# Kernel optimization log

Measured on AMD Instinct MI355X. Metric: run time of the kernel, lower is better.

The kernel has to match this reference:

```python
import jax, jax.numpy as jnp
import numpy as np

N_NODES = 100000


def _gcn_layer(x, src, dst, W, b, n_nodes):
    # x: [N, Cin]; src/dst already include self-loops
    h = x @ W  # [N, Cout]
    deg = jax.ops.segment_sum(jnp.ones_like(dst, dtype=h.dtype), dst,
                              num_segments=n_nodes)  # in-degree incl. self-loop
    dinv = jnp.where(deg > 0, deg ** -0.5, 0.0)
    norm = dinv[src] * dinv[dst]  # [E]
    msg = h[src] * norm[:, None]  # [E, Cout]
    out = jax.ops.segment_sum(msg, dst, num_segments=n_nodes)
    return out + b


def setup_inputs() -> dict:
    key = jax.random.key(0)
    k1, k2, k3, k4, k5, k6, k7 = jax.random.split(key, 7)
    E = 6400000
    x = jax.random.normal(k1, (N_NODES, 5), dtype=jnp.float32)
    edge_index = jax.random.randint(k2, (2, E), 0, N_NODES, dtype=jnp.int64)
    edge_f = jax.random.normal(k3, (E,), dtype=jnp.float32)
    edge_attr = jax.random.normal(k4, (E, 1), dtype=jnp.float32)
    # GCNConv params (glorot-ish scale)
    W1 = jax.random.normal(k5, (5, 8), dtype=jnp.float32) * (1.0 / np.sqrt(5))
    b1 = jnp.zeros((8,), dtype=jnp.float32)
    W2 = jax.random.normal(k6, (8, 5), dtype=jnp.float32) * (1.0 / np.sqrt(8))
    b2 = jnp.zeros((5,), dtype=jnp.float32)
    return {"x": x, "edge_index": edge_index, "edge_f": edge_f,
            "edge_attr": edge_attr, "W1": W1, "b1": b1, "W2": W2, "b2": b2}


def reference(x, edge_index, edge_f, edge_attr, W1, b1, W2, b2):
    n = x.shape[0]
    loops = jnp.arange(n, dtype=edge_index.dtype)
    src = jnp.concatenate([edge_index[0], loops])  # add self-loops (PyG default)
    dst = jnp.concatenate([edge_index[1], loops])
    h = _gcn_layer(x, src, dst, W1, b1, n)
    h = _gcn_layer(h, src, dst, W2, b2, n)
    return h
```

## Files before the change

### kernel.cpp

```cpp
#include <hip/hip_runtime.h>
#include <hip/hip_fp16.h>


#define TPB 256
#define VPB 256
#define B_BITS 8
#define MAXB 512
#define CAP 17408
#define NBLK_E 512
#define EPB 12500
#define SCT 512

typedef int int4e __attribute__((ext_vector_type(4)));
typedef _Float16 h8 __attribute__((ext_vector_type(8)));

__device__ __forceinline__ int4e ntload4(const int* p) {
    return __builtin_nontemporal_load((const int4e*)p);
}
__device__ __forceinline__ int ntload(const int* p) {
    return __builtin_nontemporal_load(p);
}

__global__ void k_init(int B, int* __restrict__ bpos) {
    int b = blockIdx.x * blockDim.x + threadIdx.x;
    if (b < B) bpos[b] = b * CAP;
}

__global__ __launch_bounds__(SCT) void k_scat(const int* __restrict__ src,
        const int* __restrict__ dst, int E, int B,
        int* __restrict__ bpos, int* __restrict__ pairs) {
    __shared__ int sorted[EPB];
    __shared__ int hist[MAXB], scn[MAXB], cur[MAXB], gbase[MAXB];
    int t = threadIdx.x;
    for (int i = t; i < MAXB; i += SCT) hist[i] = 0;
    __syncthreads();
    int lo = blockIdx.x * EPB;
    int n = min(E - lo, EPB);
    int n4 = n & ~3;
    for (int i = t * 4; i < n4; i += SCT * 4) {
        int4e d4 = ntload4(dst + lo + i);
        atomicAdd(&hist[d4.x >> B_BITS], 1);
        atomicAdd(&hist[d4.y >> B_BITS], 1);
        atomicAdd(&hist[d4.z >> B_BITS], 1);
        atomicAdd(&hist[d4.w >> B_BITS], 1);
    }
    for (int i = n4 + t; i < n; i += SCT)
        atomicAdd(&hist[dst[lo + i] >> B_BITS], 1);
    __syncthreads();
    if (t < MAXB) scn[t] = hist[t];
    __syncthreads();
    for (int off = 1; off < MAXB; off <<= 1) {
        int v = (t >= off && t < MAXB) ? scn[t - off] : 0;
        __syncthreads();
        if (t < MAXB) scn[t] += v;
        __syncthreads();
    }
    if (t < MAXB) {
        int h = hist[t];
        cur[t] = scn[t] - h;
        gbase[t] = (t < B && h) ? atomicAdd(&bpos[t], h) : 0;
    }
    __syncthreads();
    for (int i = t * 4; i < n4; i += SCT * 4) {
        int4e d4 = ntload4(dst + lo + i);
        int4e s4 = ntload4(src + lo + i);
        int p;
        p = atomicAdd(&cur[d4.x >> B_BITS], 1); sorted[p] = (s4.x << B_BITS) | (d4.x & (VPB - 1));
        p = atomicAdd(&cur[d4.y >> B_BITS], 1); sorted[p] = (s4.y << B_BITS) | (d4.y & (VPB - 1));
        p = atomicAdd(&cur[d4.z >> B_BITS], 1); sorted[p] = (s4.z << B_BITS) | (d4.z & (VPB - 1));
        p = atomicAdd(&cur[d4.w >> B_BITS], 1); sorted[p] = (s4.w << B_BITS) | (d4.w & (VPB - 1));
    }
    for (int i = n4 + t; i < n; i += SCT) {
        int d = dst[lo + i], s = src[lo + i];
        int p = atomicAdd(&cur[d >> B_BITS], 1);
        sorted[p] = (s << B_BITS) | (d & (VPB - 1));
    }
    __syncthreads();
    int wave = t >> 6, lane = t & 63;
    for (int bb = wave; bb < B; bb += (SCT >> 6)) {
        int h = hist[bb];
        int st = scn[bb] - h;
        int gb = gbase[bb];
        for (int j = lane; j < h; j += 64)
            pairs[gb + j] = sorted[st + j];
    }
}

__global__ __launch_bounds__(1024) void k_pre(int* __restrict__ pairs,
        const int* __restrict__ bpos, const float* __restrict__ x,
        unsigned int* __restrict__ jinfo, _Float16* __restrict__ xs, int N) {
    __shared__ int csr[CAP];
    __shared__ int hist[VPB], cur[VPB];
    __shared__ int scn[VPB];
    int t = threadIdx.x, b = blockIdx.x;
    if (t < VPB) hist[t] = 0;
    __syncthreads();
    int base = b * CAP;
    int n = bpos[b] - base, n4 = n & ~3;
    for (int i = t * 4; i < n4; i += 1024 * 4) {
        int4e p = ntload4(pairs + base + i);
        atomicAdd(&hist[p.x & (VPB - 1)], 1);
        atomicAdd(&hist[p.y & (VPB - 1)], 1);
        atomicAdd(&hist[p.z & (VPB - 1)], 1);
        atomicAdd(&hist[p.w & (VPB - 1)], 1);
    }
    for (int i = n4 + t; i < n; i += 1024)
        atomicAdd(&hist[pairs[base + i] & (VPB - 1)], 1);
    __syncthreads();
    if (t < VPB) scn[t] = hist[t];
    __syncthreads();
    for (int off = 1; off < VPB; off <<= 1) {
        int v = (t >= off && t < VPB) ? scn[t - off] : 0;
        __syncthreads();
        if (t < VPB) scn[t] += v;
        __syncthreads();
    }
    int node = b * VPB + t;
    if (t < VPB) {
        int h = hist[t];
        int sl = scn[t] - h;
        cur[t] = sl;
        if (node < N) {
            jinfo[node] = ((unsigned int)(base + sl) << 9) | (unsigned int)h;
            float di = rsqrtf((float)(h + 1));
            const float* xp = x + (size_t)node * 5;
            h8 v;
            v[0] = (_Float16)(xp[0] * di); v[1] = (_Float16)(xp[1] * di);
            v[2] = (_Float16)(xp[2] * di); v[3] = (_Float16)(xp[3] * di);
            v[4] = (_Float16)(xp[4] * di);
            v[5] = (_Float16)0.f; v[6] = (_Float16)0.f; v[7] = (_Float16)0.f;
            *(h8*)(xs + (size_t)node * 8) = v;
        }
    }
    __syncthreads();
    for (int i = t * 4; i < n4; i += 1024 * 4) {
        int4e p = ntload4(pairs + base + i);
        int q;
        q = atomicAdd(&cur[p.x & (VPB - 1)], 1); csr[q] = p.x >> B_BITS;
        q = atomicAdd(&cur[p.y & (VPB - 1)], 1); csr[q] = p.y >> B_BITS;
        q = atomicAdd(&cur[p.z & (VPB - 1)], 1); csr[q] = p.z >> B_BITS;
        q = atomicAdd(&cur[p.w & (VPB - 1)], 1); csr[q] = p.w >> B_BITS;
    }
    for (int i = n4 + t; i < n; i += 1024) {
        int p = pairs[base + i];
        int q = atomicAdd(&cur[p & (VPB - 1)], 1);
        csr[q] = p >> B_BITS;
    }
    __syncthreads();
    for (int i = t; i < n; i += 1024)
        __builtin_nontemporal_store(csr[i], pairs + base + i);
}

__global__ __launch_bounds__(TPB) void k_g1(const int* __restrict__ pairs,
        const unsigned int* __restrict__ jinfo, const _Float16* __restrict__ xs,
        const float* __restrict__ W1, const float* __restrict__ b1,
        const float* __restrict__ W2, _Float16* __restrict__ h2s, int N) {
    int gid = blockIdx.x * blockDim.x + threadIdx.x;
    int node = gid >> 3, lane = gid & 7;
    if (node >= N) return;
    unsigned int u = jinfo[node];
    int jsa = (int)(u >> 9), cn = (int)(u & 511u);
    float a0 = 0.f, a1 = 0.f, a2 = 0.f, a3 = 0.f, a4 = 0.f;
    int j = lane;
    for (; j + 24 < cn; j += 32) {
        int sA = ntload(pairs + jsa + j);
        int sB = ntload(pairs + jsa + j + 8);
        int sC = ntload(pairs + jsa + j + 16);
        int sD = ntload(pairs + jsa + j + 24);
        h8 vA = *(const h8*)(xs + (size_t)sA * 8);
        h8 vB = *(const h8*)(xs + (size_t)sB * 8);
        h8 vC = *(const h8*)(xs + (size_t)sC * 8);
        h8 vD = *(const h8*)(xs + (size_t)sD * 8);
        a0 += (float)vA[0] + (float)vB[0] + (float)vC[0] + (float)vD[0];
        a1 += (float)vA[1] + (float)vB[1] + (float)vC[1] + (float)vD[1];
        a2 += (float)vA[2] + (float)vB[2] + (float)vC[2] + (float)vD[2];
        a3 += (float)vA[3] + (float)vB[3] + (float)vC[3] + (float)vD[3];
        a4 += (float)vA[4] + (float)vB[4] + (float)vC[4] + (float)vD[4];
    }
    for (; j < cn; j += 8) {
        int sA = ntload(pairs + jsa + j);
        h8 vA = *(const h8*)(xs + (size_t)sA * 8);
        a0 += (float)vA[0]; a1 += (float)vA[1]; a2 += (float)vA[2];
        a3 += (float)vA[3]; a4 += (float)vA[4];
    }
#pragma unroll
    for (int d = 1; d < 8; d <<= 1) {
        a0 += __shfl_xor(a0, d); a1 += __shfl_xor(a1, d);
        a2 += __shfl_xor(a2, d); a3 += __shfl_xor(a3, d);
        a4 += __shfl_xor(a4, d);
    }
    float di = rsqrtf((float)(cn + 1));
    h8 sv = *(const h8*)(xs + (size_t)node * 8);
    float tc[5];
    tc[0] = a0 + (float)sv[0]; tc[1] = a1 + (float)sv[1];
    tc[2] = a2 + (float)sv[2]; tc[3] = a3 + (float)sv[3];
    tc[4] = a4 + (float)sv[4];
    float o1[8];
#pragma unroll
    for (int jj = 0; jj < 8; ++jj) {
        float h = 0.f;
#pragma unroll
        for (int c = 0; c < 5; ++c) h += tc[c] * W1[c * 8 + jj];
        o1[jj] = h * di + b1[jj];
    }
    if (lane == 0) {
        h8 w;
#pragma unroll
        for (int k = 0; k < 5; ++k) {
            float h = 0.f;
#pragma unroll
            for (int jj = 0; jj < 8; ++jj) h += o1[jj] * W2[jj * 5 + k];
            w[k] = (_Float16)(h * di);
        }
        w[5] = (_Float16)0.f; w[6] = (_Float16)0.f; w[7] = (_Float16)0.f;
        *(h8*)(h2s + (size_t)node * 8) = w;
    }
}

__global__ __launch_bounds__(TPB) void k_g2(const int* __restrict__ pairs,
        const unsigned int* __restrict__ jinfo, const _Float16* __restrict__ h2s,
        const float* __restrict__ b2, float* __restrict__ out, int N) {
    int gid = blockIdx.x * blockDim.x + threadIdx.x;
    int node = gid >> 3, lane = gid & 7;
    if (node >= N) return;
    unsigned int u = jinfo[node];
    int jsa = (int)(u >> 9), cn = (int)(u & 511u);
    float a0 = 0.f, a1 = 0.f, a2 = 0.f, a3 = 0.f, a4 = 0.f;
    int j = lane;
    for (; j + 24 < cn; j += 32) {
        int sA = ntload(pairs + jsa + j);
        int sB = ntload(pairs + jsa + j + 8);
        int sC = ntload(pairs + jsa + j + 16);
        int sD = ntload(pairs + jsa + j + 24);
        h8 vA = *(const h8*)(h2s + (size_t)sA * 8);
        h8 vB = *(const h8*)(h2s + (size_t)sB * 8);
        h8 vC = *(const h8*)(h2s + (size_t)sC * 8);
        h8 vD = *(const h8*)(h2s + (size_t)sD * 8);
        a0 += (float)vA[0] + (float)vB[0] + (float)vC[0] + (float)vD[0];
        a1 += (float)vA[1] + (float)vB[1] + (float)vC[1] + (float)vD[1];
        a2 += (float)vA[2] + (float)vB[2] + (float)vC[2] + (float)vD[2];
        a3 += (float)vA[3] + (float)vB[3] + (float)vC[3] + (float)vD[3];
        a4 += (float)vA[4] + (float)vB[4] + (float)vC[4] + (float)vD[4];
    }
    for (; j < cn; j += 8) {
        int sA = ntload(pairs + jsa + j);
        h8 vA = *(const h8*)(h2s + (size_t)sA * 8);
        a0 += (float)vA[0]; a1 += (float)vA[1]; a2 += (float)vA[2];
        a3 += (float)vA[3]; a4 += (float)vA[4];
    }
#pragma unroll
    for (int d = 1; d < 8; d <<= 1) {
        a0 += __shfl_xor(a0, d); a1 += __shfl_xor(a1, d);
        a2 += __shfl_xor(a2, d); a3 += __shfl_xor(a3, d);
        a4 += __shfl_xor(a4, d);
    }
    if (lane == 0) {
        float di = rsqrtf((float)(cn + 1));
        h8 sv = *(const h8*)(h2s + (size_t)node * 8);
        float* op = out + (size_t)node * 5;
        op[0] = (a0 + (float)sv[0]) * di + b2[0];
        op[1] = (a1 + (float)sv[1]) * di + b2[1];
        op[2] = (a2 + (float)sv[2]) * di + b2[2];
        op[3] = (a3 + (float)sv[3]) * di + b2[3];
        op[4] = (a4 + (float)sv[4]) * di + b2[4];
    }
}

extern "C" void kernel_launch(void* const* d_in, const int* in_sizes, int n_in,
                              void* d_out, int out_size, void* d_ws, size_t ws_size,
                              hipStream_t stream) {
    const float* x   = (const float*)d_in[0];
    const int*  eidx = (const int*)d_in[1];
    const float* W1 = (const float*)d_in[4];
    const float* b1 = (const float*)d_in[5];
    const float* W2 = (const float*)d_in[6];
    const float* b2 = (const float*)d_in[7];
    float* out = (float*)d_out;

    const int N = in_sizes[0] / 5;
    const int E = in_sizes[1] / 2;
    const int* src = eidx;
    const int* dst = eidx + E;

    const int B = (N + VPB - 1) / VPB;

    int*      pairs = (int*)d_ws;
    _Float16* xs    = (_Float16*)(pairs + (size_t)B * CAP);
    _Float16* h2s   = xs + (size_t)8 * N;
    unsigned int* jinfo = (unsigned int*)(h2s + (size_t)8 * N);
    int*      bpos  = (int*)(jinfo + N);

    const int g8N = (8 * N + TPB - 1) / TPB;

    k_init <<<(B + TPB - 1) / TPB, TPB, 0, stream>>>(B, bpos);
    k_scat <<<NBLK_E, SCT, 0, stream>>>(src, dst, E, B, bpos, pairs);
    k_pre  <<<B, 1024, 0, stream>>>(pairs, bpos, x, jinfo, xs, N);
    k_g1   <<<g8N, TPB, 0, stream>>>(pairs, jinfo, xs, W1, b1, W2, h2s, N);
    k_g2   <<<g8N, TPB, 0, stream>>>(pairs, jinfo, h2s, b2, out, N);
}
```

Measured before the change: 255.4 us.

## Drop nontemporal hints, prefetch gather indices, and remap blocks to interleave node buckets

```diff
diff --git a/kernel.cpp b/kernel.cpp
--- a/kernel.cpp
+++ b/kernel.cpp
@@ -14,11 +14,8 @@
 typedef int int4e __attribute__((ext_vector_type(4)));
 typedef _Float16 h8 __attribute__((ext_vector_type(8)));
 
-__device__ __forceinline__ int4e ntload4(const int* p) {
-    return __builtin_nontemporal_load((const int4e*)p);
-}
-__device__ __forceinline__ int ntload(const int* p) {
-    return __builtin_nontemporal_load(p);
+__device__ __forceinline__ int4e ld4(const int* p) {
+    return *(const int4e*)p;
 }
 
 __global__ void k_init(int B, int* __restrict__ bpos) {
@@ -38,7 +35,7 @@
     int n = min(E - lo, EPB);
     int n4 = n & ~3;
     for (int i = t * 4; i < n4; i += SCT * 4) {
-        int4e d4 = ntload4(dst + lo + i);
+        int4e d4 = ld4(dst + lo + i);
         atomicAdd(&hist[d4.x >> B_BITS], 1);
         atomicAdd(&hist[d4.y >> B_BITS], 1);
         atomicAdd(&hist[d4.z >> B_BITS], 1);
@@ -62,8 +59,8 @@
     }
     __syncthreads();
     for (int i = t * 4; i < n4; i += SCT * 4) {
-        int4e d4 = ntload4(dst + lo + i);
-        int4e s4 = ntload4(src + lo + i);
+        int4e d4 = ld4(dst + lo + i);
+        int4e s4 = ld4(src + lo + i);
         int p;
         p = atomicAdd(&cur[d4.x >> B_BITS], 1); sorted[p] = (s4.x << B_BITS) | (d4.x & (VPB - 1));
         p = atomicAdd(&cur[d4.y >> B_BITS], 1); sorted[p] = (s4.y << B_BITS) | (d4.y & (VPB - 1));
@@ -98,7 +95,7 @@
     int base = b * CAP;
     int n = bpos[b] - base, n4 = n & ~3;
     for (int i = t * 4; i < n4; i += 1024 * 4) {
-        int4e p = ntload4(pairs + base + i);
+        int4e p = ld4(pairs + base + i);
         atomicAdd(&hist[p.x & (VPB - 1)], 1);
         atomicAdd(&hist[p.y & (VPB - 1)], 1);
         atomicAdd(&hist[p.z & (VPB - 1)], 1);
@@ -134,7 +131,7 @@
     }
     __syncthreads();
     for (int i = t * 4; i < n4; i += 1024 * 4) {
-        int4e p = ntload4(pairs + base + i);
+        int4e p = ld4(pairs + base + i);
         int q;
         q = atomicAdd(&cur[p.x & (VPB - 1)], 1); csr[q] = p.x >> B_BITS;
         q = atomicAdd(&cur[p.y & (VPB - 1)], 1); csr[q] = p.y >> B_BITS;
@@ -148,37 +145,55 @@
     }
     __syncthreads();
     for (int i = t; i < n; i += 1024)
-        __builtin_nontemporal_store(csr[i], pairs + base + i);
+        pairs[base + i] = csr[i];
+}
+
+__device__ __forceinline__ void g_map(int g, int t, int* node, int* lane) {
+    int q = g >> 6, r = g & 63;
+    int b = q * 8 + (r & 7);
+    int s = r >> 3;
+    *node = b * VPB + s * 32 + (t >> 3);
+    *lane = t & 7;
 }
 
 __global__ __launch_bounds__(TPB) void k_g1(const int* __restrict__ pairs,
         const unsigned int* __restrict__ jinfo, const _Float16* __restrict__ xs,
         const float* __restrict__ W1, const float* __restrict__ b1,
         const float* __restrict__ W2, _Float16* __restrict__ h2s, int N) {
-    int gid = blockIdx.x * blockDim.x + threadIdx.x;
-    int node = gid >> 3, lane = gid & 7;
+    int node, lane;
+    g_map(blockIdx.x, threadIdx.x, &node, &lane);
     if (node >= N) return;
     unsigned int u = jinfo[node];
     int jsa = (int)(u >> 9), cn = (int)(u & 511u);
     float a0 = 0.f, a1 = 0.f, a2 = 0.f, a3 = 0.f, a4 = 0.f;
     int j = lane;
-    for (; j + 24 < cn; j += 32) {
-        int sA = ntload(pairs + jsa + j);
-        int sB = ntload(pairs + jsa + j + 8);
-        int sC = ntload(pairs + jsa + j + 16);
-        int sD = ntload(pairs + jsa + j + 24);
-        h8 vA = *(const h8*)(xs + (size_t)sA * 8);
-        h8 vB = *(const h8*)(xs + (size_t)sB * 8);
-        h8 vC = *(const h8*)(xs + (size_t)sC * 8);
-        h8 vD = *(const h8*)(xs + (size_t)sD * 8);
-        a0 += (float)vA[0] + (float)vB[0] + (float)vC[0] + (float)vD[0];
-        a1 += (float)vA[1] + (float)vB[1] + (float)vC[1] + (float)vD[1];
-        a2 += (float)vA[2] + (float)vB[2] + (float)vC[2] + (float)vD[2];
-        a3 += (float)vA[3] + (float)vB[3] + (float)vC[3] + (float)vD[3];
-        a4 += (float)vA[4] + (float)vB[4] + (float)vC[4] + (float)vD[4];
+    if (j + 24 < cn) {
+        int iA = pairs[jsa + j],      iB = pairs[jsa + j + 8];
+        int iC = pairs[jsa + j + 16], iD = pairs[jsa + j + 24];
+        for (;;) {
+            int nj = j + 32;
+            bool more = (nj + 24 < cn);
+            int pA, pB, pC, pD;
+            if (more) {
+                pA = pairs[jsa + nj];      pB = pairs[jsa + nj + 8];
+                pC = pairs[jsa + nj + 16]; pD = pairs[jsa + nj + 24];
+            }
+            h8 vA = *(const h8*)(xs + (size_t)iA * 8);
+            h8 vB = *(const h8*)(xs + (size_t)iB * 8);
+            h8 vC = *(const h8*)(xs + (size_t)iC * 8);
+            h8 vD = *(const h8*)(xs + (size_t)iD * 8);
+            a0 += (float)vA[0] + (float)vB[0] + (float)vC[0] + (float)vD[0];
+            a1 += (float)vA[1] + (float)vB[1] + (float)vC[1] + (float)vD[1];
+            a2 += (float)vA[2] + (float)vB[2] + (float)vC[2] + (float)vD[2];
+            a3 += (float)vA[3] + (float)vB[3] + (float)vC[3] + (float)vD[3];
+            a4 += (float)vA[4] + (float)vB[4] + (float)vC[4] + (float)vD[4];
+            if (!more) break;
+            iA = pA; iB = pB; iC = pC; iD = pD; j = nj;
+        }
+        j += 32;
     }
     for (; j < cn; j += 8) {
-        int sA = ntload(pairs + jsa + j);
+        int sA = pairs[jsa + j];
         h8 vA = *(const h8*)(xs + (size_t)sA * 8);
         a0 += (float)vA[0]; a1 += (float)vA[1]; a2 += (float)vA[2];
         a3 += (float)vA[3]; a4 += (float)vA[4];
@@ -220,30 +235,40 @@
 __global__ __launch_bounds__(TPB) void k_g2(const int* __restrict__ pairs,
         const unsigned int* __restrict__ jinfo, const _Float16* __restrict__ h2s,
         const float* __restrict__ b2, float* __restrict__ out, int N) {
-    int gid = blockIdx.x * blockDim.x + threadIdx.x;
-    int node = gid >> 3, lane = gid & 7;
+    int node, lane;
+    g_map(blockIdx.x, threadIdx.x, &node, &lane);
     if (node >= N) return;
     unsigned int u = jinfo[node];
     int jsa = (int)(u >> 9), cn = (int)(u & 511u);
     float a0 = 0.f, a1 = 0.f, a2 = 0.f, a3 = 0.f, a4 = 0.f;
     int j = lane;
-    for (; j + 24 < cn; j += 32) {
-        int sA = ntload(pairs + jsa + j);
-        int sB = ntload(pairs + jsa + j + 8);
-        int sC = ntload(pairs + jsa + j + 16);
-        int sD = ntload(pairs + jsa + j + 24);
-        h8 vA = *(const h8*)(h2s + (size_t)sA * 8);
-        h8 vB = *(const h8*)(h2s + (size_t)sB * 8);
-        h8 vC = *(const h8*)(h2s + (size_t)sC * 8);
-        h8 vD = *(const h8*)(h2s + (size_t)sD * 8);
-        a0 += (float)vA[0] + (float)vB[0] + (float)vC[0] + (float)vD[0];
-        a1 += (float)vA[1] + (float)vB[1] + (float)vC[1] + (float)vD[1];
-        a2 += (float)vA[2] + (float)vB[2] + (float)vC[2] + (float)vD[2];
-        a3 += (float)vA[3] + (float)vB[3] + (float)vC[3] + (float)vD[3];
-        a4 += (float)vA[4] + (float)vB[4] + (float)vC[4] + (float)vD[4];
+    if (j + 24 < cn) {
+        int iA = pairs[jsa + j],      iB = pairs[jsa + j + 8];
+        int iC = pairs[jsa + j + 16], iD = pairs[jsa + j + 24];
+        for (;;) {
+            int nj = j + 32;
+            bool more = (nj + 24 < cn);
+            int pA, pB, pC, pD;
+            if (more) {
+                pA = pairs[jsa + nj];      pB = pairs[jsa + nj + 8];
+                pC = pairs[jsa + nj + 16]; pD = pairs[jsa + nj + 24];
+            }
+            h8 vA = *(const h8*)(h2s + (size_t)iA * 8);
+            h8 vB = *(const h8*)(h2s + (size_t)iB * 8);
+            h8 vC = *(const h8*)(h2s + (size_t)iC * 8);
+            h8 vD = *(const h8*)(h2s + (size_t)iD * 8);
+            a0 += (float)vA[0] + (float)vB[0] + (float)vC[0] + (float)vD[0];
+            a1 += (float)vA[1] + (float)vB[1] + (float)vC[1] + (float)vD[1];
+            a2 += (float)vA[2] + (float)vB[2] + (float)vC[2] + (float)vD[2];
+            a3 += (float)vA[3] + (float)vB[3] + (float)vC[3] + (float)vD[3];
+            a4 += (float)vA[4] + (float)vB[4] + (float)vC[4] + (float)vD[4];
+            if (!more) break;
+            iA = pA; iB = pB; iC = pC; iD = pD; j = nj;
+        }
+        j += 32;
     }
     for (; j < cn; j += 8) {
-        int sA = ntload(pairs + jsa + j);
+        int sA = pairs[jsa + j];
         h8 vA = *(const h8*)(h2s + (size_t)sA * 8);
         a0 += (float)vA[0]; a1 += (float)vA[1]; a2 += (float)vA[2];
         a3 += (float)vA[3]; a4 += (float)vA[4];
@@ -290,11 +315,11 @@
     unsigned int* jinfo = (unsigned int*)(h2s + (size_t)8 * N);
     int*      bpos  = (int*)(jinfo + N);
 
-    const int g8N = (8 * N + TPB - 1) / TPB;
+    const int gG = ((B + 7) / 8) * 64;
 
     k_init <<<(B + TPB - 1) / TPB, TPB, 0, stream>>>(B, bpos);
     k_scat <<<NBLK_E, SCT, 0, stream>>>(src, dst, E, B, bpos, pairs);
     k_pre  <<<B, 1024, 0, stream>>>(pairs, bpos, x, jinfo, xs, N);
-    k_g1   <<<g8N, TPB, 0, stream>>>(pairs, jinfo, xs, W1, b1, W2, h2s, N);
-    k_g2   <<<g8N, TPB, 0, stream>>>(pairs, jinfo, h2s, b2, out, N);
-}
+    k_g1   <<<gG, TPB, 0, stream>>>(pairs, jinfo, xs, W1, b1, W2, h2s, N);
+    k_g2   <<<gG, TPB, 0, stream>>>(pairs, jinfo, h2s, b2, out, N);
+}
```

Result: faster. 227.4 us (-11.0%).
